# Kernel optimization log

Measured on AMD Instinct MI355X. Metric: run time of the kernel, lower is better.

Reference implementation:

```python
import jax, jax.numpy as jnp
import numpy as np

B, Q, C = 64, 512, 128   # batch, num_queries, num_activity_classes
P, G = 2048, 256         # num_persons, num_target_groups
COST_BCE = 1.0
COST_ACT = 1.0


def setup_inputs() -> dict:
    key = jax.random.key(0)
    k1, k2, k3, k4 = jax.random.split(key, 4)
    pred_activity_logits = jax.random.normal(k1, (B, Q, C), dtype=jnp.float32)
    attention_weights = jax.random.normal(k2, (B, P, Q), dtype=jnp.float32)
    # binary one-hot-style grouping targets (~each person in 1-of-G groups; sparse 0/1)
    tgt_one_hot = (jax.random.uniform(k3, (B, P, G)) < (1.0 / G) * 8).astype(jnp.float32)
    tgt_activity_ids = jax.random.randint(k4, (B, G), 0, C, dtype=jnp.int64)
    return {
        "pred_activity_logits": pred_activity_logits,
        "attention_weights": attention_weights,
        "tgt_one_hot": tgt_one_hot,
        "tgt_activity_ids": tgt_activity_ids,
    }


def reference(pred_activity_logits, attention_weights, tgt_one_hot, tgt_activity_ids):
    """Fused cost-matrix computation.

    BCEWithLogits(x, t) (mean reduction) = mean(softplus(x) - x * t).
    grouping_cost[b,i,j] = mean_p BCE(attw[b,p,i], onehot[b,p,j])
                         = mean_p softplus(attw[b,p,i]) - (1/P) sum_p attw[b,p,i]*onehot[b,p,j]
    activity_cost[b,i,j] = mean_c BCE(logits[b,i,c], onehot(ids[b,j])[c])
                         = mean_c softplus(logits[b,i,c]) - (1/C) * logits[b,i,ids[b,j]]
    Returns the [B, Q, G] cost tensor (scipy linear_sum_assignment, which consumes
    it on CPU, is outside the kernel scope).
    """
    attw = attention_weights            # [B, P, Q]
    logits = pred_activity_logits       # [B, Q, C]
    p = attw.shape[1]
    c = logits.shape[2]

    # grouping (BCE) cost
    sp_g = jnp.mean(jax.nn.softplus(attw), axis=1)               # [B, Q]
    xt = jnp.einsum('bpq,bpg->bqg', attw, tgt_one_hot) / p       # [B, Q, G]
    grouping_cost = sp_g[:, :, None] - xt                        # [B, Q, G]

    # activity (BCE vs one-hot class) cost
    sp_a = jnp.mean(jax.nn.softplus(logits), axis=2)             # [B, Q]
    idx = jnp.broadcast_to(tgt_activity_ids[:, None, :], (logits.shape[0], logits.shape[1], tgt_activity_ids.shape[1]))
    gathered = jnp.take_along_axis(logits, idx.astype(jnp.int32), axis=2)  # [B, Q, G]
    activity_cost = sp_a[:, :, None] - gathered / c              # [B, Q, G]

    cost = COST_BCE * grouping_cost + COST_ACT * activity_cost
    return cost
```

## Files before the change

### kernel.cpp

```cpp
#include <hip/hip_runtime.h>
#include <hip/hip_bf16.h>

#define B_  64
#define Q_  512
#define C_  128
#define P_  2048
#define G_  256
#define BM  128
#define BN  256
#define BK  64
#define NT  512
#define NTILES (P_ / BK)
#define HALF ((BM + BN) * BK)

typedef __attribute__((ext_vector_type(8))) short short8;
typedef __attribute__((ext_vector_type(4))) float floatx4;

union FragU { uint4 u; short8 s; };

__device__ __forceinline__ float bf2f(unsigned short h) {
    union { unsigned int i; float f; } v; v.i = ((unsigned int)h) << 16; return v.f;
}
__device__ __forceinline__ unsigned int fbits(float f) {
    union { float f; unsigned int u; } v; v.f = f; return v.u;
}
__device__ __forceinline__ unsigned int f2bf(float f) {
    unsigned int u = fbits(f);
    return (u + 0x7FFFu + ((u >> 16) & 1u)) >> 16;
}
__device__ __forceinline__ float splus(float x) {
    return fmaxf(x, 0.f) + __logf(1.f + __expf(-fabsf(x)));
}
__device__ __forceinline__ void unpack8(float4 a, float4 b, float* c) {
    c[0] = a.x; c[1] = a.y; c[2] = a.z; c[3] = a.w;
    c[4] = b.x; c[5] = b.y; c[6] = b.z; c[7] = b.w;
}

__device__ __forceinline__ void barrier_lds_only() {
    asm volatile("s_waitcnt lgkmcnt(0)" ::: "memory");
    __builtin_amdgcn_s_barrier();
    asm volatile("" ::: "memory");
}

__global__ __launch_bounds__(NT, 2)
void fused_cost_kernel(const float* __restrict__ logits,
                       const float* __restrict__ attw,
                       const float* __restrict__ onehot,
                       const int* __restrict__ ids,
                       float* __restrict__ out)
{
    __shared__ unsigned short smem[2 * HALF];
    __shared__ float spq[BM];
    __shared__ int idt[BN];
    __shared__ int sflags;

    const int tid = threadIdx.x;
    const int l   = tid & 63;
    const int w   = tid >> 6;
    const int wm  = w & 1;
    const int wn  = w >> 1;
    const int lm  = l & 15;
    const int lk  = l >> 4;

    const int nb = blockIdx.x * BN;
    const int mb = blockIdx.y * BM;
    const int b  = blockIdx.z;

    if (tid < BM) spq[tid] = 0.f;
    if (tid == 0) sflags = 0;
    __syncthreads();
    if (tid < 128) { if (ids[2 * tid + 1] != 0) atomicOr(&sflags, 1); }
    __syncthreads();
    const bool ids32 = (sflags & 1) != 0;
    if (tid < BN) {
        const int gidx = b * G_ + nb + tid;
        idt[tid] = ids32 ? ids[gidx] : ids[2 * gidx];
    }

    const int mvA = tid & 15;
    const int kqA = tid >> 4;
    const int hbA = kqA >> 2;
    const int kdA = kqA & 3;
    const int mvB = tid & 31;
    const int kqB = tid >> 5;
    const int hbB = kqB >> 1;
    const int sdB = (kqB & 1) * 4;

    const float* aBase = attw   + (size_t)b * P_ * Q_ + (size_t)(2 * kqA) * Q_ + (mb + 8 * mvA);
    const float* bBase = onehot + (size_t)b * P_ * G_ + (size_t)(4 * kqB) * G_ + (nb + 8 * mvB);

    float spacc[8] = {0.f, 0.f, 0.f, 0.f, 0.f, 0.f, 0.f, 0.f};
    floatx4 acc[4][4];
    #pragma unroll
    for (int mi = 0; mi < 4; ++mi)
        #pragma unroll
        for (int ni = 0; ni < 4; ++ni)
            acc[mi][ni] = (floatx4){0.f, 0.f, 0.f, 0.f};

    float4 rA0 = *(const float4*)(aBase);
    float4 rA1 = *(const float4*)(aBase + 4);
    float4 rA2 = *(const float4*)(aBase + Q_);
    float4 rA3 = *(const float4*)(aBase + Q_ + 4);
    float4 rB0 = *(const float4*)(bBase);
    float4 rB1 = *(const float4*)(bBase + 4);
    float4 rB2 = *(const float4*)(bBase + G_);
    float4 rB3 = *(const float4*)(bBase + G_ + 4);
    float4 rB4 = *(const float4*)(bBase + 2 * G_);
    float4 rB5 = *(const float4*)(bBase + 2 * G_ + 4);
    float4 rB6 = *(const float4*)(bBase + 3 * G_);
    float4 rB7 = *(const float4*)(bBase + 3 * G_ + 4);

    #pragma unroll 2
    for (int t = 0; t < NTILES; ++t) {
        unsigned short* As = smem + (t & 1) * HALF;
        unsigned short* Bs = As + BM * BK;

        {
            float c0[8], c1[8];
            unpack8(rA0, rA1, c0);
            unpack8(rA2, rA3, c1);
            #pragma unroll
            for (int j = 0; j < 8; ++j) {
                spacc[j] += splus(c0[j]) + splus(c1[j]);
                const unsigned int d = f2bf(c0[j]) | (f2bf(c1[j]) << 16);
                const int m  = 8 * mvA + j;
                const int sw = (m + (m >> 3)) & 7;
                *(unsigned int*)(&As[m * BK + ((hbA ^ sw) << 3) + 2 * kdA]) = d;
            }
        }
        {
            float c0[8], c1[8], c2[8], c3[8];
            unpack8(rB0, rB1, c0);
            unpack8(rB2, rB3, c1);
            unpack8(rB4, rB5, c2);
            unpack8(rB6, rB7, c3);
            #pragma unroll
            for (int j = 0; j < 8; ++j) {
                uint2 dv;
                dv.x = (fbits(c0[j]) >> 16) | (fbits(c1[j]) & 0xFFFF0000u);
                dv.y = (fbits(c2[j]) >> 16) | (fbits(c3[j]) & 0xFFFF0000u);
                const int n  = 8 * mvB + j;
                const int sw = (n + (n >> 3)) & 7;
                *(uint2*)(&Bs[n * BK + ((hbB ^ sw) << 3) + sdB]) = dv;
            }
        }
        if (t + 1 < NTILES) {
            const float* an = aBase + (size_t)(t + 1) * BK * Q_;
            const float* bn = bBase + (size_t)(t + 1) * BK * G_;
            rA0 = *(const float4*)(an);
            rA1 = *(const float4*)(an + 4);
            rA2 = *(const float4*)(an + Q_);
            rA3 = *(const float4*)(an + Q_ + 4);
            rB0 = *(const float4*)(bn);
            rB1 = *(const float4*)(bn + 4);
            rB2 = *(const float4*)(bn + G_);
            rB3 = *(const float4*)(bn + G_ + 4);
            rB4 = *(const float4*)(bn + 2 * G_);
            rB5 = *(const float4*)(bn + 2 * G_ + 4);
            rB6 = *(const float4*)(bn + 3 * G_);
            rB7 = *(const float4*)(bn + 3 * G_ + 4);
        }
        barrier_lds_only();

        #pragma unroll
        for (int s = 0; s < 2; ++s) {
            FragU a4[4], b4[4];
            #pragma unroll
            for (int mi = 0; mi < 4; ++mi) {
                const int m  = 64 * wm + 16 * mi + lm;
                const int sw = (m + (m >> 3)) & 7;
                a4[mi].u = *(const uint4*)(&As[m * BK + (((4 * s + lk) ^ sw) << 3)]);
            }
            #pragma unroll
            for (int ni = 0; ni < 4; ++ni) {
                const int n  = 64 * wn + 16 * ni + lm;
                const int sw = (n + (n >> 3)) & 7;
                b4[ni].u = *(const uint4*)(&Bs[n * BK + (((4 * s + lk) ^ sw) << 3)]);
            }
            #pragma unroll
            for (int mi = 0; mi < 4; ++mi)
                #pragma unroll
                for (int ni = 0; ni < 4; ++ni)
                    acc[mi][ni] = __builtin_amdgcn_mfma_f32_16x16x32_bf16(
                        a4[mi].s, b4[ni].s, acc[mi][ni], 0, 0, 0);
        }
    }

    #pragma unroll
    for (int j = 0; j < 8; ++j)
        atomicAdd(&spq[8 * mvA + j], spacc[j] * (1.0f / P_));

    __syncthreads();

    {
        const int q  = tid >> 2;
        const int qt = tid & 3;
        const float4* src = (const float4*)(logits + ((size_t)b * Q_ + (mb + q)) * C_ + 32 * qt);
        uint2* dst = (uint2*)(&smem[q * C_ + 32 * qt]);
        float ssum = 0.f;
        #pragma unroll
        for (int i = 0; i < 8; ++i) {
            float4 t = src[i];
            ssum += splus(t.x) + splus(t.y) + splus(t.z) + splus(t.w);
            uint2 dv;
            dv.x = f2bf(t.x) | (f2bf(t.y) << 16);
            dv.y = f2bf(t.z) | (f2bf(t.w) << 16);
            dst[i] = dv;
        }
        atomicAdd(&spq[q], ssum * (1.0f / C_));
    }
    __syncthreads();

    float* outp = out + ((size_t)b * Q_ + mb) * G_ + nb;
    #pragma unroll
    for (int mi = 0; mi < 4; ++mi) {
        const int q0 = 64 * wm + 16 * mi + 4 * lk;
        #pragma unroll
        for (int ni = 0; ni < 4; ++ni) {
            const int g   = 64 * wn + 16 * ni + lm;
            const int cid = idt[g];
            #pragma unroll
            for (int r = 0; r < 4; ++r) {
                const int q = q0 + r;
                const float val = spq[q]
                                - acc[mi][ni][r] * (1.0f / P_)
                                - bf2f(smem[q * C_ + cid]) * (1.0f / C_);
                outp[(size_t)q * G_ + g] = val;
            }
        }
    }
}

extern "C" void kernel_launch(void* const* d_in, const int* in_sizes, int n_in,
                              void* d_out, int out_size, void* d_ws, size_t ws_size,
                              hipStream_t stream) {
    const float* logits = (const float*)d_in[0];
    const float* attw   = (const float*)d_in[1];
    const float* onehot = (const float*)d_in[2];
    const int*   ids    = (const int*)d_in[3];
    float*       out    = (float*)d_out;

    dim3 grid(G_ / BN, Q_ / BM, B_);
    hipLaunchKernelGGL(fused_cost_kernel, grid, dim3(NT), 0, stream,
                       logits, attw, onehot, ids, out);
}
```

Before: 474.6 us.

## Reshape block tile to 256x64 with single-buffered LDS and higher occupancy

Changes the output tile from 128x256 to 256x64 per block. The thread-to-data mapping for both operand loaders is reworked, only half the threads load the one-hot operand, and the warp grid becomes 4x2. The double-buffered LDS staging is replaced by a single buffer with an extra barrier per K step, and launch bounds now ask for 4 blocks per CU. The intent is more blocks in flight to hide latency, but attention weights are now re-read and their softplus recomputed by every N-block, which raises global traffic and redundant transcendental work.

```diff
diff --git a/kernel.cpp b/kernel.cpp
--- a/kernel.cpp
+++ b/kernel.cpp
@@ -6,12 +6,11 @@
 #define C_  128
 #define P_  2048
 #define G_  256
-#define BM  128
-#define BN  256
+#define BM  256
+#define BN  64
 #define BK  64
 #define NT  512
 #define NTILES (P_ / BK)
-#define HALF ((BM + BN) * BK)
 
 typedef __attribute__((ext_vector_type(8))) short short8;
 typedef __attribute__((ext_vector_type(4))) float floatx4;
@@ -42,23 +41,25 @@
     asm volatile("" ::: "memory");
 }
 
-__global__ __launch_bounds__(NT, 2)
+__global__ __launch_bounds__(NT, 4)
 void fused_cost_kernel(const float* __restrict__ logits,
                        const float* __restrict__ attw,
                        const float* __restrict__ onehot,
                        const int* __restrict__ ids,
                        float* __restrict__ out)
 {
-    __shared__ unsigned short smem[2 * HALF];
+    __shared__ unsigned short smem[BM * C_];
     __shared__ float spq[BM];
     __shared__ int idt[BN];
     __shared__ int sflags;
+    unsigned short* As = smem;
+    unsigned short* Bs = smem + BM * BK;
 
     const int tid = threadIdx.x;
     const int l   = tid & 63;
     const int w   = tid >> 6;
-    const int wm  = w & 1;
-    const int wn  = w >> 1;
+    const int wm  = w & 3;
+    const int wn  = w >> 2;
     const int lm  = l & 15;
     const int lk  = l >> 4;
 
@@ -77,94 +78,97 @@
         idt[tid] = ids32 ? ids[gidx] : ids[2 * gidx];
     }
 
-    const int mvA = tid & 15;
-    const int kqA = tid >> 4;
-    const int hbA = kqA >> 2;
-    const int kdA = kqA & 3;
-    const int mvB = tid & 31;
-    const int kqB = tid >> 5;
-    const int hbB = kqB >> 1;
-    const int sdB = (kqB & 1) * 4;
-
-    const float* aBase = attw   + (size_t)b * P_ * Q_ + (size_t)(2 * kqA) * Q_ + (mb + 8 * mvA);
-    const float* bBase = onehot + (size_t)b * P_ * G_ + (size_t)(4 * kqB) * G_ + (nb + 8 * mvB);
+    const int mvA = tid & 31;
+    const int kqA = tid >> 5;
+    const int hbA = kqA >> 1;
+    const int sdA = (kqA & 1) * 4;
+    const int mvB = tid & 7;
+    const int kqB = (tid & 255) >> 3;
+    const int hbB = kqB >> 2;
+    const int kdB = kqB & 3;
+    const bool doB = (tid < 256);
+
+    const float* aBase = attw   + (size_t)b * P_ * Q_ + (size_t)(4 * kqA) * Q_ + (mb + 8 * mvA);
+    const float* bBase = onehot + (size_t)b * P_ * G_ + (size_t)(2 * kqB) * G_ + (nb + 8 * mvB);
 
     float spacc[8] = {0.f, 0.f, 0.f, 0.f, 0.f, 0.f, 0.f, 0.f};
-    floatx4 acc[4][4];
+    floatx4 acc[4][2];
     #pragma unroll
     for (int mi = 0; mi < 4; ++mi)
         #pragma unroll
-        for (int ni = 0; ni < 4; ++ni)
+        for (int ni = 0; ni < 2; ++ni)
             acc[mi][ni] = (floatx4){0.f, 0.f, 0.f, 0.f};
 
     float4 rA0 = *(const float4*)(aBase);
     float4 rA1 = *(const float4*)(aBase + 4);
     float4 rA2 = *(const float4*)(aBase + Q_);
     float4 rA3 = *(const float4*)(aBase + Q_ + 4);
-    float4 rB0 = *(const float4*)(bBase);
-    float4 rB1 = *(const float4*)(bBase + 4);
-    float4 rB2 = *(const float4*)(bBase + G_);
-    float4 rB3 = *(const float4*)(bBase + G_ + 4);
-    float4 rB4 = *(const float4*)(bBase + 2 * G_);
-    float4 rB5 = *(const float4*)(bBase + 2 * G_ + 4);
-    float4 rB6 = *(const float4*)(bBase + 3 * G_);
-    float4 rB7 = *(const float4*)(bBase + 3 * G_ + 4);
-
-    #pragma unroll 2
+    float4 rA4 = *(const float4*)(aBase + 2 * Q_);
+    float4 rA5 = *(const float4*)(aBase + 2 * Q_ + 4);
+    float4 rA6 = *(const float4*)(aBase + 3 * Q_);
+    float4 rA7 = *(const float4*)(aBase + 3 * Q_ + 4);
+    float4 rB0, rB1, rB2, rB3;
+    if (doB) {
+        rB0 = *(const float4*)(bBase);
+        rB1 = *(const float4*)(bBase + 4);
+        rB2 = *(const float4*)(bBase + G_);
+        rB3 = *(const float4*)(bBase + G_ + 4);
+    }
+
     for (int t = 0; t < NTILES; ++t) {
-        unsigned short* As = smem + (t & 1) * HALF;
-        unsigned short* Bs = As + BM * BK;
-
         {
-            float c0[8], c1[8];
+            float c0[8], c1[8], c2[8], c3[8];
             unpack8(rA0, rA1, c0);
             unpack8(rA2, rA3, c1);
+            unpack8(rA4, rA5, c2);
+            unpack8(rA6, rA7, c3);
             #pragma unroll
             for (int j = 0; j < 8; ++j) {
-                spacc[j] += splus(c0[j]) + splus(c1[j]);
-                const unsigned int d = f2bf(c0[j]) | (f2bf(c1[j]) << 16);
+                spacc[j] += (splus(c0[j]) + splus(c1[j]))
+                          + (splus(c2[j]) + splus(c3[j]));
+                uint2 dv;
+                dv.x = f2bf(c0[j]) | (f2bf(c1[j]) << 16);
+                dv.y = f2bf(c2[j]) | (f2bf(c3[j]) << 16);
                 const int m  = 8 * mvA + j;
                 const int sw = (m + (m >> 3)) & 7;
-                *(unsigned int*)(&As[m * BK + ((hbA ^ sw) << 3) + 2 * kdA]) = d;
-            }
-        }
-        {
-            float c0[8], c1[8], c2[8], c3[8];
+                *(uint2*)(&As[m * BK + ((hbA ^ sw) << 3) + sdA]) = dv;
+            }
+        }
+        if (doB) {
+            float c0[8], c1[8];
             unpack8(rB0, rB1, c0);
             unpack8(rB2, rB3, c1);
-            unpack8(rB4, rB5, c2);
-            unpack8(rB6, rB7, c3);
             #pragma unroll
             for (int j = 0; j < 8; ++j) {
-                uint2 dv;
-                dv.x = (fbits(c0[j]) >> 16) | (fbits(c1[j]) & 0xFFFF0000u);
-                dv.y = (fbits(c2[j]) >> 16) | (fbits(c3[j]) & 0xFFFF0000u);
+                const unsigned int d = (fbits(c0[j]) >> 16) | (fbits(c1[j]) & 0xFFFF0000u);
                 const int n  = 8 * mvB + j;
                 const int sw = (n + (n >> 3)) & 7;
-                *(uint2*)(&Bs[n * BK + ((hbB ^ sw) << 3) + sdB]) = dv;
+                *(unsigned int*)(&Bs[n * BK + ((hbB ^ sw) << 3) + 2 * kdB]) = d;
             }
         }
         if (t + 1 < NTILES) {
             const float* an = aBase + (size_t)(t + 1) * BK * Q_;
-            const float* bn = bBase + (size_t)(t + 1) * BK * G_;
             rA0 = *(const float4*)(an);
             rA1 = *(const float4*)(an + 4);
             rA2 = *(const float4*)(an + Q_);
             rA3 = *(const float4*)(an + Q_ + 4);
-            rB0 = *(const float4*)(bn);
-            rB1 = *(const float4*)(bn + 4);
-            rB2 = *(const float4*)(bn + G_);
-            rB3 = *(const float4*)(bn + G_ + 4);
-            rB4 = *(const float4*)(bn + 2 * G_);
-            rB5 = *(const float4*)(bn + 2 * G_ + 4);
-            rB6 = *(const float4*)(bn + 3 * G_);
-            rB7 = *(const float4*)(bn + 3 * G_ + 4);
+            rA4 = *(const float4*)(an + 2 * Q_);
+            rA5 = *(const float4*)(an + 2 * Q_ + 4);
+            rA6 = *(const float4*)(an + 3 * Q_);
+            rA7 = *(const float4*)(an + 3 * Q_ + 4);
+            if (doB) {
+                const float* bn = bBase + (size_t)(t + 1) * BK * G_;
+                rB0 = *(const float4*)(bn);
+                rB1 = *(const float4*)(bn + 4);
+                rB2 = *(const float4*)(bn + G_);
+                rB3 = *(const float4*)(bn + G_ + 4);
+            }
         }
         barrier_lds_only();
 
         #pragma unroll
         for (int s = 0; s < 2; ++s) {
-            FragU a4[4], b4[4];
+            FragU a4[4], b4[2];
             #pragma unroll
             for (int mi = 0; mi < 4; ++mi) {
                 const int m  = 64 * wm + 16 * mi + lm;
@@ -172,18 +176,19 @@
                 a4[mi].u = *(const uint4*)(&As[m * BK + (((4 * s + lk) ^ sw) << 3)]);
             }
             #pragma unroll
-            for (int ni = 0; ni < 4; ++ni) {
-                const int n  = 64 * wn + 16 * ni + lm;
+            for (int ni = 0; ni < 2; ++ni) {
+                const int n  = 32 * wn + 16 * ni + lm;
                 const int sw = (n + (n >> 3)) & 7;
                 b4[ni].u = *(const uint4*)(&Bs[n * BK + (((4 * s + lk) ^ sw) << 3)]);
             }
             #pragma unroll
             for (int mi = 0; mi < 4; ++mi)
                 #pragma unroll
-                for (int ni = 0; ni < 4; ++ni)
+                for (int ni = 0; ni < 2; ++ni)
                     acc[mi][ni] = __builtin_amdgcn_mfma_f32_16x16x32_bf16(
                         a4[mi].s, b4[ni].s, acc[mi][ni], 0, 0, 0);
         }
+        barrier_lds_only();
     }
 
     #pragma unroll
@@ -193,13 +198,13 @@
     __syncthreads();
 
     {
-        const int q  = tid >> 2;
-        const int qt = tid & 3;
-        const float4* src = (const float4*)(logits + ((size_t)b * Q_ + (mb + q)) * C_ + 32 * qt);
-        uint2* dst = (uint2*)(&smem[q * C_ + 32 * qt]);
+        const int q  = tid >> 1;
+        const int qh = tid & 1;
+        const float4* src = (const float4*)(logits + ((size_t)b * Q_ + (mb + q)) * C_ + 64 * qh);
+        uint2* dst = (uint2*)(&smem[q * C_ + 64 * qh]);
         float ssum = 0.f;
         #pragma unroll
-        for (int i = 0; i < 8; ++i) {
+        for (int i = 0; i < 16; ++i) {
             float4 t = src[i];
             ssum += splus(t.x) + splus(t.y) + splus(t.z) + splus(t.w);
             uint2 dv;
@@ -216,8 +221,8 @@
     for (int mi = 0; mi < 4; ++mi) {
         const int q0 = 64 * wm + 16 * mi + 4 * lk;
         #pragma unroll
-        for (int ni = 0; ni < 4; ++ni) {
-            const int g   = 64 * wn + 16 * ni + lm;
+        for (int ni = 0; ni < 2; ++ni) {
+            const int g   = 32 * wn + 16 * ni + lm;
             const int cid = idt[g];
             #pragma unroll
             for (int r = 0; r < 4; ++r) {
```

Result: slower. 836.1 us (+76.2%).
